# Kernel optimization log

Measured on AMD Instinct MI355X. Metric: run time of the kernel, lower is better.

Reference implementation:

```python
import jax, jax.numpy as jnp
from jax import lax
import numpy as np

# Geometry fixed by __init__ (see shape_source)
UP = 2          # up_factor[0]
DOWN = 2        # down_factor[0]
PAD_LO = 11
PAD_HI = 10
SLOPE = 0.2
GAIN = np.sqrt(2.0).astype(np.float32)


def _kaiser_beta(atten):
    if atten > 50:
        return 0.1102 * (atten - 8.7)
    if atten > 21:
        return 0.5842 * (atten - 21.0) ** 0.4 + 0.07886 * (atten - 21.0)
    return 0.0


def _firwin(numtaps, cutoff, width, fs):
    # numpy re-implementation of scipy.signal.firwin(numtaps, cutoff, width=width, fs=fs)
    nyq = fs / 2.0
    atten = 2.285 * (numtaps - 1) * np.pi * (width / nyq) + 7.95  # kaiser_atten
    beta = _kaiser_beta(atten)
    m = np.arange(numtaps) - (numtaps - 1) / 2.0
    fc = cutoff / nyq
    h = fc * np.sinc(fc * m) * np.kaiser(numtaps, beta)
    h = h / h.sum()  # unity DC gain (pass_zero scaling)
    return h.astype(np.float32)


def _depthwise_conv1d(x, f, axis, stride=1, lhs_dilation=1, padding=(0, 0)):
    """Depthwise 1D FIR along spatial `axis` (2 or 3) of NCHW tensor.
    Filter is flipped (true convolution, as in upfirdn2d)."""
    C = x.shape[1]
    k = f.shape[0]
    fr = f[::-1]
    if axis == 2:
        kern = jnp.broadcast_to(fr.reshape(1, 1, k, 1), (C, 1, k, 1))
        strides, ld, pads = (stride, 1), (lhs_dilation, 1), [padding, (0, 0)]
    else:
        kern = jnp.broadcast_to(fr.reshape(1, 1, 1, k), (C, 1, 1, k))
        strides, ld, pads = (1, stride), (1, lhs_dilation), [(0, 0), padding]
    return lax.conv_general_dilated(
        x, kern, window_strides=strides, padding=pads, lhs_dilation=ld,
        dimension_numbers=('NCHW', 'OIHW', 'NCHW'), feature_group_count=C)


def setup_inputs() -> dict:
    key = jax.random.key(0)
    k1, k2 = jax.random.split(key)
    x = jax.random.normal(k1, (32, 128, 64, 64), dtype=jnp.float32)
    bias = jax.random.normal(k2, (128,), dtype=jnp.float32) * 0.1
    # up filter: numtaps=12, cutoff=in_cutoff=28, width=2*in_half_width=8, fs=tmp_sr=128
    up_filter = jnp.asarray(_firwin(12, 28.0, 8.0, 128.0))
    # down filter: numtaps=12, cutoff=out_cutoff=28, width=2*out_half_width=8, fs=128
    down_filter = jnp.asarray(_firwin(12, 28.0, 8.0, 128.0))
    return {"x": x, "bias": bias, "up_filter": up_filter, "down_filter": down_filter}


def reference(x, bias, up_filter, down_filter):
    # filtered_lrelu reference: upfirdn2d(up, fu, gain=up**2) -> bias -> lrelu*sqrt(2) -> upfirdn2d(down, fd)
    # Zero-insertion upsampling fused via lhs_dilation; dilated length is H*UP-(UP-1),
    # so the trailing UP-1 zeros of the nominal H*UP upsampled signal move into pad_hi.
    fu = up_filter * UP  # gain up per separable pass -> up**2 total
    pad = (PAD_LO, PAD_HI + UP - 1)
    y = _depthwise_conv1d(x, fu, axis=2, lhs_dilation=UP, padding=pad)
    y = _depthwise_conv1d(y, fu, axis=3, lhs_dilation=UP, padding=pad)  # [B,C,138,138]
    y = y + bias[None, :, None, None]
    y = jnp.where(y >= 0, y, SLOPE * y) * GAIN
    y = _depthwise_conv1d(y, down_filter, axis=2, stride=DOWN)
    y = _depthwise_conv1d(y, down_filter, axis=3, stride=DOWN)  # [B,C,64,64]
    return y
```

## Files before the change

kernel.cpp:

```cpp
#include <hip/hip_runtime.h>


#define NT 1024
#define SLOPE 0.2f
#define GAIN 1.41421356237309504880f

#define XROWS 43
#define XSTRIDE 68
#define ZROWS 74
#define ZSTRIDE 84
#define ZPAD 8
#define YROWS 74
#define YSTRIDE 148
#define WSTRIDE 140

#define XB_OFF 0
#define ZB_OFF (XROWS * XSTRIDE)
#define WB_OFF 0
#define YB_OFF (ZB_OFF + ZROWS * ZSTRIDE)
#define LDS_FLOATS (YB_OFF + YROWS * YSTRIDE)

__global__ __launch_bounds__(NT, 8) void fused_upfirdn_lrelu(
    const float* __restrict__ x,
    const float* __restrict__ bias,
    const float* __restrict__ upf,
    const float* __restrict__ dnf,
    float* __restrict__ out)
{
    extern __shared__ float lds[];
    float* xb = lds + XB_OFF;
    float* zb = lds + ZB_OFF;
    float* wb = lds + WB_OFF;
    float* yb = lds + YB_OFF;

    const int t = threadIdx.x;
    const int bid = blockIdx.x;
    const int s = bid >> 1;
    const int o0 = (bid & 1) << 5;
    const int c = s & 127;
    const int xlo = o0 - 5;

    float fu[12], fd[12];
#pragma unroll
    for (int j = 0; j < 12; ++j) { fu[j] = 2.0f * upf[j]; fd[j] = dnf[j]; }
    const float bv = bias[c];

    const float* xg = x + (size_t)s * 4096;
    float* og = out + (size_t)s * 4096;

    for (int task = t; task < XROWS * 16; task += NT) {
        const int rl = task >> 4;
        const int c4 = (task & 15) << 2;
        const int r = xlo + rl;
        float4 v = make_float4(0.f, 0.f, 0.f, 0.f);
        if (r >= 0 && r <= 63) v = *reinterpret_cast<const float4*>(xg + r * 64 + c4);
        *reinterpret_cast<float4*>(xb + rl * XSTRIDE + c4) = v;
    }
    for (int task = t; task < ZROWS * 5; task += NT) {
        const int rl = task / 5;
        const int p = task - rl * 5;
        const int col = (p < 2) ? (p << 2) : (72 + ((p - 2) << 2));
        *reinterpret_cast<float4*>(zb + rl * ZSTRIDE + col) = make_float4(0.f, 0.f, 0.f, 0.f);
    }
    __syncthreads();

    for (int task = t; task < 19 * 16; task += NT) {
        const int k = task >> 4;
        const int c4 = (task & 15) << 2;
        const float* xr = xb + (2 * k) * XSTRIDE + c4;
        float4 xv[7];
#pragma unroll
        for (int r = 0; r < 7; ++r) xv[r] = *reinterpret_cast<const float4*>(xr + r * XSTRIDE);
        float a0[4] = {0,0,0,0}, a1[4] = {0,0,0,0}, b0[4] = {0,0,0,0}, b1[4] = {0,0,0,0};
#pragma unroll
        for (int d = 0; d < 6; ++d) {
            const float w0 = fu[2 * (5 - d)], w1 = fu[2 * (5 - d) + 1];
            a0[0] += w0 * xv[d].x; a0[1] += w0 * xv[d].y; a0[2] += w0 * xv[d].z; a0[3] += w0 * xv[d].w;
            a1[0] += w1 * xv[d].x; a1[1] += w1 * xv[d].y; a1[2] += w1 * xv[d].z; a1[3] += w1 * xv[d].w;
        }
#pragma unroll
        for (int d = 1; d < 7; ++d) {
            const float w0 = fu[2 * (6 - d)], w1 = fu[2 * (6 - d) + 1];
            b0[0] += w0 * xv[d].x; b0[1] += w0 * xv[d].y; b0[2] += w0 * xv[d].z; b0[3] += w0 * xv[d].w;
            b1[0] += w1 * xv[d].x; b1[1] += w1 * xv[d].y; b1[2] += w1 * xv[d].z; b1[3] += w1 * xv[d].w;
        }
        float* zr = zb + (4 * k) * ZSTRIDE + ZPAD + c4;
        *reinterpret_cast<float4*>(zr)               = make_float4(a0[0], a0[1], a0[2], a0[3]);
        *reinterpret_cast<float4*>(zr + ZSTRIDE)     = make_float4(a1[0], a1[1], a1[2], a1[3]);
        if (k < 18) {
            *reinterpret_cast<float4*>(zr + 2 * ZSTRIDE) = make_float4(b0[0], b0[1], b0[2], b0[3]);
            *reinterpret_cast<float4*>(zr + 3 * ZSTRIDE) = make_float4(b1[0], b1[1], b1[2], b1[3]);
        }
    }
    __syncthreads();

    for (int task = t; task < YROWS * 9; task += NT) {
        const int il = task / 9;
        const int m8 = task - il * 9;
        const int mbase = m8 << 3;
        const float* zr = zb + il * ZSTRIDE + mbase;
        float zv[16];
#pragma unroll
        for (int q = 0; q < 4; ++q) {
            const float4 v = *reinterpret_cast<const float4*>(zr + (q << 2));
            zv[4 * q] = v.x; zv[4 * q + 1] = v.y; zv[4 * q + 2] = v.z; zv[4 * q + 3] = v.w;
        }
        float yv[16];
#pragma unroll
        for (int e = 0; e < 8; ++e) {
            float a0 = 0.0f, a1 = 0.0f;
#pragma unroll
            for (int tt = 0; tt < 6; ++tt) {
                const float zz = zv[8 + e - tt];
                a0 += fu[2 * tt]     * zz;
                a1 += fu[2 * tt + 1] * zz;
            }
            a0 += bv; a1 += bv;
            a0 = (a0 >= 0.0f ? a0 : SLOPE * a0) * GAIN;
            a1 = (a1 >= 0.0f ? a1 : SLOPE * a1) * GAIN;
            yv[2 * e] = a0; yv[2 * e + 1] = a1;
        }
        float* yr = yb + il * YSTRIDE + (mbase << 1);
#pragma unroll
        for (int q = 0; q < 4; ++q)
            *reinterpret_cast<float4*>(yr + (q << 2)) =
                make_float4(yv[4 * q], yv[4 * q + 1], yv[4 * q + 2], yv[4 * q + 3]);
    }
    __syncthreads();

    for (int task = t; task < 8 * 35; task += NT) {
        const int og = task / 35;
        const int col4 = (task - og * 35) << 2;
        const float* yr = yb + (og << 3) * YSTRIDE + col4;
        float acc[4][4] = {{0,0,0,0},{0,0,0,0},{0,0,0,0},{0,0,0,0}};
#pragma unroll
        for (int r = 0; r < 18; ++r) {
            const float4 v = *reinterpret_cast<const float4*>(yr + r * YSTRIDE);
#pragma unroll
            for (int e = 0; e < 4; ++e) {
                if (r >= 2 * e && r <= 2 * e + 11) {
                    const float w = fd[11 - r + 2 * e];
                    acc[e][0] += w * v.x; acc[e][1] += w * v.y;
                    acc[e][2] += w * v.z; acc[e][3] += w * v.w;
                }
            }
        }
        float* wr = wb + (og << 2) * WSTRIDE + col4;
#pragma unroll
        for (int e = 0; e < 4; ++e)
            *reinterpret_cast<float4*>(wr + e * WSTRIDE) =
                make_float4(acc[e][0], acc[e][1], acc[e][2], acc[e][3]);
    }
    __syncthreads();

    for (int task = t; task < 32 * 8; task += NT) {
        const int ol = task >> 3;
        const int ow8 = task & 7;
        const float* wr = wb + ol * WSTRIDE + (ow8 << 4);
        float wv[28];
#pragma unroll
        for (int q = 0; q < 7; ++q) {
            const float4 v = *reinterpret_cast<const float4*>(wr + (q << 2));
            wv[4 * q] = v.x; wv[4 * q + 1] = v.y; wv[4 * q + 2] = v.z; wv[4 * q + 3] = v.w;
        }
        float rv[8];
#pragma unroll
        for (int e = 0; e < 8; ++e) {
            float a = 0.0f;
#pragma unroll
            for (int j = 0; j < 12; ++j) a += fd[j] * wv[2 * e + 11 - j];
            rv[e] = a;
        }
        float* orow = og + (o0 + ol) * 64 + (ow8 << 3);
        *reinterpret_cast<float4*>(orow)     = make_float4(rv[0], rv[1], rv[2], rv[3]);
        *reinterpret_cast<float4*>(orow + 4) = make_float4(rv[4], rv[5], rv[6], rv[7]);
    }
}

extern "C" void kernel_launch(void* const* d_in, const int* in_sizes, int n_in,
                              void* d_out, int out_size, void* d_ws, size_t ws_size,
                              hipStream_t stream) {
    const float* x    = (const float*)d_in[0];
    const float* bias = (const float*)d_in[1];
    const float* upf  = (const float*)d_in[2];
    const float* dnf  = (const float*)d_in[3];
    float* out = (float*)d_out;

    const int n_blocks = 32 * 128 * 2;
    const size_t lds_bytes = (size_t)LDS_FLOATS * sizeof(float);
    hipLaunchKernelGGL(fused_upfirdn_lrelu, dim3(n_blocks), dim3(NT),
                       lds_bytes, stream, x, bias, upf, dnf, out);
}
```

Before: 85.62 us.

## Load x directly from global and reorder downsample passes to horizontal-first

Drops the x staging buffer in LDS and its barrier, so the vertical upsample threads read input rows straight from global memory, while other threads zero the pad columns at the same time. The downsample order is swapped: the horizontal pass runs first on all 74 rows and writes a 74x64 intermediate, then the vertical pass writes directly to global output. Work is also remapped to thread-index ranges in column-major order. The aim is less LDS traffic, one fewer barrier and a smaller buffer, at the cost of more horizontal downsample work (74 rows instead of 32) and more redundant global reads of overlapping x rows.

```diff
diff --git a/kernel.cpp b/kernel.cpp
--- a/kernel.cpp
+++ b/kernel.cpp
@@ -5,19 +5,16 @@
 #define SLOPE 0.2f
 #define GAIN 1.41421356237309504880f
 
-#define XROWS 43
-#define XSTRIDE 68
 #define ZROWS 74
 #define ZSTRIDE 84
 #define ZPAD 8
 #define YROWS 74
 #define YSTRIDE 148
-#define WSTRIDE 140
+#define YWSTRIDE 68
 
-#define XB_OFF 0
-#define ZB_OFF (XROWS * XSTRIDE)
-#define WB_OFF 0
-#define YB_OFF (ZB_OFF + ZROWS * ZSTRIDE)
+#define ZB_OFF 0
+#define YB_OFF (ZROWS * ZSTRIDE)
+#define YW_OFF 0
 #define LDS_FLOATS (YB_OFF + YROWS * YSTRIDE)
 
 __global__ __launch_bounds__(NT, 8) void fused_upfirdn_lrelu(
@@ -28,17 +25,15 @@
     float* __restrict__ out)
 {
     extern __shared__ float lds[];
-    float* xb = lds + XB_OFF;
     float* zb = lds + ZB_OFF;
-    float* wb = lds + WB_OFF;
     float* yb = lds + YB_OFF;
+    float* yw = lds + YW_OFF;
 
     const int t = threadIdx.x;
     const int bid = blockIdx.x;
     const int s = bid >> 1;
     const int o0 = (bid & 1) << 5;
     const int c = s & 127;
-    const int xlo = o0 - 5;
 
     float fu[12], fd[12];
 #pragma unroll
@@ -46,31 +41,21 @@
     const float bv = bias[c];
 
     const float* xg = x + (size_t)s * 4096;
-    float* og = out + (size_t)s * 4096;
+    float* outg = out + (size_t)s * 4096;
 
-    for (int task = t; task < XROWS * 16; task += NT) {
-        const int rl = task >> 4;
-        const int c4 = (task & 15) << 2;
-        const int r = xlo + rl;
-        float4 v = make_float4(0.f, 0.f, 0.f, 0.f);
-        if (r >= 0 && r <= 63) v = *reinterpret_cast<const float4*>(xg + r * 64 + c4);
-        *reinterpret_cast<float4*>(xb + rl * XSTRIDE + c4) = v;
-    }
-    for (int task = t; task < ZROWS * 5; task += NT) {
-        const int rl = task / 5;
-        const int p = task - rl * 5;
-        const int col = (p < 2) ? (p << 2) : (72 + ((p - 2) << 2));
-        *reinterpret_cast<float4*>(zb + rl * ZSTRIDE + col) = make_float4(0.f, 0.f, 0.f, 0.f);
-    }
-    __syncthreads();
-
-    for (int task = t; task < 19 * 16; task += NT) {
-        const int k = task >> 4;
-        const int c4 = (task & 15) << 2;
-        const float* xr = xb + (2 * k) * XSTRIDE + c4;
+    if (t < 304) {
+        const int k = t >> 4;
+        const int c4 = (t & 15) << 2;
+        const int rbase = o0 - 5 + 2 * k;
         float4 xv[7];
 #pragma unroll
-        for (int r = 0; r < 7; ++r) xv[r] = *reinterpret_cast<const float4*>(xr + r * XSTRIDE);
+        for (int d = 0; d < 7; ++d) {
+            const int r = rbase + d;
+            if (r >= 0 && r <= 63)
+                xv[d] = *reinterpret_cast<const float4*>(xg + r * 64 + c4);
+            else
+                xv[d] = make_float4(0.f, 0.f, 0.f, 0.f);
+        }
         float a0[4] = {0,0,0,0}, a1[4] = {0,0,0,0}, b0[4] = {0,0,0,0}, b1[4] = {0,0,0,0};
 #pragma unroll
         for (int d = 0; d < 6; ++d) {
@@ -91,89 +76,98 @@
             *reinterpret_cast<float4*>(zr + 2 * ZSTRIDE) = make_float4(b0[0], b0[1], b0[2], b0[3]);
             *reinterpret_cast<float4*>(zr + 3 * ZSTRIDE) = make_float4(b1[0], b1[1], b1[2], b1[3]);
         }
+    } else if (t < 674) {
+        const int pt = t - 304;
+        const int rl = pt / 5;
+        const int p = pt - rl * 5;
+        const int col = (p < 2) ? (p << 2) : (72 + ((p - 2) << 2));
+        *reinterpret_cast<float4*>(zb + rl * ZSTRIDE + col) = make_float4(0.f, 0.f, 0.f, 0.f);
     }
     __syncthreads();
 
-    for (int task = t; task < YROWS * 9; task += NT) {
-        const int il = task / 9;
-        const int m8 = task - il * 9;
-        const int mbase = m8 << 3;
-        const float* zr = zb + il * ZSTRIDE + mbase;
-        float zv[16];
+    if (t < 720) {
+        const int m8 = t / 80;
+        const int il = t - m8 * 80;
+        if (il < YROWS) {
+            const int mbase = m8 << 3;
+            const float* zr = zb + il * ZSTRIDE + mbase;
+            float zv[16];
 #pragma unroll
-        for (int q = 0; q < 4; ++q) {
-            const float4 v = *reinterpret_cast<const float4*>(zr + (q << 2));
-            zv[4 * q] = v.x; zv[4 * q + 1] = v.y; zv[4 * q + 2] = v.z; zv[4 * q + 3] = v.w;
+            for (int q = 0; q < 4; ++q) {
+                const float4 v = *reinterpret_cast<const float4*>(zr + (q << 2));
+                zv[4 * q] = v.x; zv[4 * q + 1] = v.y; zv[4 * q + 2] = v.z; zv[4 * q + 3] = v.w;
+            }
+            float yv[16];
+#pragma unroll
+            for (int e = 0; e < 8; ++e) {
+                float a0 = 0.0f, a1 = 0.0f;
+#pragma unroll
+                for (int tt = 0; tt < 6; ++tt) {
+                    const float zz = zv[8 + e - tt];
+                    a0 += fu[2 * tt]     * zz;
+                    a1 += fu[2 * tt + 1] * zz;
+                }
+                a0 += bv; a1 += bv;
+                a0 = (a0 >= 0.0f ? a0 : SLOPE * a0) * GAIN;
+                a1 = (a1 >= 0.0f ? a1 : SLOPE * a1) * GAIN;
+                yv[2 * e] = a0; yv[2 * e + 1] = a1;
+            }
+            float* yr = yb + il * YSTRIDE + (mbase << 1);
+#pragma unroll
+            for (int q = 0; q < 4; ++q)
+                *reinterpret_cast<float4*>(yr + (q << 2)) =
+                    make_float4(yv[4 * q], yv[4 * q + 1], yv[4 * q + 2], yv[4 * q + 3]);
         }
-        float yv[16];
-#pragma unroll
-        for (int e = 0; e < 8; ++e) {
-            float a0 = 0.0f, a1 = 0.0f;
-#pragma unroll
-            for (int tt = 0; tt < 6; ++tt) {
-                const float zz = zv[8 + e - tt];
-                a0 += fu[2 * tt]     * zz;
-                a1 += fu[2 * tt + 1] * zz;
-            }
-            a0 += bv; a1 += bv;
-            a0 = (a0 >= 0.0f ? a0 : SLOPE * a0) * GAIN;
-            a1 = (a1 >= 0.0f ? a1 : SLOPE * a1) * GAIN;
-            yv[2 * e] = a0; yv[2 * e + 1] = a1;
-        }
-        float* yr = yb + il * YSTRIDE + (mbase << 1);
-#pragma unroll
-        for (int q = 0; q < 4; ++q)
-            *reinterpret_cast<float4*>(yr + (q << 2)) =
-                make_float4(yv[4 * q], yv[4 * q + 1], yv[4 * q + 2], yv[4 * q + 3]);
     }
     __syncthreads();
 
-    for (int task = t; task < 8 * 35; task += NT) {
-        const int og = task / 35;
-        const int col4 = (task - og * 35) << 2;
-        const float* yr = yb + (og << 3) * YSTRIDE + col4;
+    if (t < 640) {
+        const int cg = t / 80;
+        const int il = t - cg * 80;
+        if (il < YROWS) {
+            const float* yr = yb + il * YSTRIDE + (cg << 4);
+            float w[28];
+#pragma unroll
+            for (int q = 0; q < 7; ++q) {
+                const float4 v = *reinterpret_cast<const float4*>(yr + (q << 2));
+                w[4 * q] = v.x; w[4 * q + 1] = v.y; w[4 * q + 2] = v.z; w[4 * q + 3] = v.w;
+            }
+            float rv[8];
+#pragma unroll
+            for (int e = 0; e < 8; ++e) {
+                float a = 0.0f;
+#pragma unroll
+                for (int j = 0; j < 12; ++j) a += fd[j] * w[2 * e + 11 - j];
+                rv[e] = a;
+            }
+            float* wr = yw + il * YWSTRIDE + (cg << 3);
+            *reinterpret_cast<float4*>(wr)     = make_float4(rv[0], rv[1], rv[2], rv[3]);
+            *reinterpret_cast<float4*>(wr + 4) = make_float4(rv[4], rv[5], rv[6], rv[7]);
+        }
+    }
+    __syncthreads();
+
+    if (t < 128) {
+        const int eg = t >> 4;
+        const int col4 = (t & 15) << 2;
+        const float* wr = yw + (eg << 3) * YWSTRIDE + col4;
         float acc[4][4] = {{0,0,0,0},{0,0,0,0},{0,0,0,0},{0,0,0,0}};
 #pragma unroll
         for (int r = 0; r < 18; ++r) {
-            const float4 v = *reinterpret_cast<const float4*>(yr + r * YSTRIDE);
+            const float4 v = *reinterpret_cast<const float4*>(wr + r * YWSTRIDE);
 #pragma unroll
             for (int e = 0; e < 4; ++e) {
                 if (r >= 2 * e && r <= 2 * e + 11) {
-                    const float w = fd[11 - r + 2 * e];
-                    acc[e][0] += w * v.x; acc[e][1] += w * v.y;
-                    acc[e][2] += w * v.z; acc[e][3] += w * v.w;
+                    const float ww = fd[11 - r + 2 * e];
+                    acc[e][0] += ww * v.x; acc[e][1] += ww * v.y;
+                    acc[e][2] += ww * v.z; acc[e][3] += ww * v.w;
                 }
             }
         }
-        float* wr = wb + (og << 2) * WSTRIDE + col4;
 #pragma unroll
         for (int e = 0; e < 4; ++e)
-            *reinterpret_cast<float4*>(wr + e * WSTRIDE) =
+            *reinterpret_cast<float4*>(outg + (o0 + (eg << 2) + e) * 64 + col4) =
                 make_float4(acc[e][0], acc[e][1], acc[e][2], acc[e][3]);
-    }
-    __syncthreads();
-
-    for (int task = t; task < 32 * 8; task += NT) {
-        const int ol = task >> 3;
-        const int ow8 = task & 7;
-        const float* wr = wb + ol * WSTRIDE + (ow8 << 4);
-        float wv[28];
-#pragma unroll
-        for (int q = 0; q < 7; ++q) {
-            const float4 v = *reinterpret_cast<const float4*>(wr + (q << 2));
-            wv[4 * q] = v.x; wv[4 * q + 1] = v.y; wv[4 * q + 2] = v.z; wv[4 * q + 3] = v.w;
-        }
-        float rv[8];
-#pragma unroll
-        for (int e = 0; e < 8; ++e) {
-            float a = 0.0f;
-#pragma unroll
-            for (int j = 0; j < 12; ++j) a += fd[j] * wv[2 * e + 11 - j];
-            rv[e] = a;
-        }
-        float* orow = og + (o0 + ol) * 64 + (ow8 << 3);
-        *reinterpret_cast<float4*>(orow)     = make_float4(rv[0], rv[1], rv[2], rv[3]);
-        *reinterpret_cast<float4*>(orow + 4) = make_float4(rv[4], rv[5], rv[6], rv[7]);
     }
 }
 
```

After: 73.72 us. 1.16x faster.
